# Performance work log

Measured on AMD Instinct MI355X. Metric: run time of the kernel, lower is better.

## Reference

```python
import jax, jax.numpy as jnp
import numpy as np


def setup_inputs() -> dict:
    key = jax.random.key(0)
    k1, k2 = jax.random.split(key)
    x = jax.random.normal(k1, (4, 4096, 128), dtype=jnp.float32)
    kernel = jax.random.normal(k2, (3, 128, 64), dtype=jnp.float32)
    return {"x": x, "kernel": kernel}


def reference(x, kernel):
    # QKV projections: x [B,N,Din] @ kernel[i] [Din,Dout] -> [B,N,Dout]
    WQ = jnp.einsum('bnd,de->bne', x, kernel[0])
    WK = jnp.einsum('bnd,de->bne', x, kernel[1])
    WV = jnp.einsum('bnd,de->bne', x, kernel[2])
    d_out = WV.shape[-1]
    # scaled dot-product scores [B,N,N]
    scores = jnp.einsum('bqe,bke->bqk', WQ, WK) / jnp.sqrt(jnp.float32(d_out))
    attn = jax.nn.softmax(scores, axis=-1)
    return jnp.einsum('bqk,bke->bqe', attn, WV)
```

## Files before the change

kernel.cpp:

```cpp
#include <hip/hip_runtime.h>


typedef __attribute__((ext_vector_type(8))) short bf16x8;
typedef __attribute__((ext_vector_type(16))) float f32x16;
typedef __attribute__((ext_vector_type(4))) unsigned u32x4;
typedef unsigned short us;

__device__ __forceinline__ us f2bf(float f) {
  unsigned u = __builtin_bit_cast(unsigned, f);
  u += 0x7FFFu + ((u >> 16) & 1u);
  return (us)(u >> 16);
}
__device__ __forceinline__ float bf2f(us h) {
  unsigned u = ((unsigned)h) << 16;
  return __builtin_bit_cast(float, u);
}
__device__ __forceinline__ f32x16 mfma(bf16x8 a, bf16x8 b, f32x16 c) {
  return __builtin_amdgcn_mfma_f32_32x32x16_bf16(a, b, c, 0, 0, 0);
}
__device__ __forceinline__ unsigned pk2t(float a, float b) {
  return __builtin_amdgcn_perm(__builtin_bit_cast(unsigned, b),
                               __builtin_bit_cast(unsigned, a), 0x07060302u);
}
__device__ __forceinline__ void dma16(const us* g, us* l) {
  __builtin_amdgcn_global_load_lds(
      (const __attribute__((address_space(1))) unsigned*)g,
      (__attribute__((address_space(3))) unsigned*)l, 16, 0, 0);
}
#define EXP2(x) __builtin_amdgcn_exp2f(x)

#define NSEG 16
#define ITERS 4

__global__ __launch_bounds__(256, 1) void wprep_kernel(
    const float* __restrict__ w, us* __restrict__ Wbh, us* __restrict__ Wbl)
{
  const int i = blockIdx.x * 256 + threadIdx.x;
  if (i >= 24576) return;
  const int p = i >> 13, d = (i & 8191) >> 6, e = i & 63;
  float v = w[i];
  if (p == 0) v *= 0.18033688011112042f;
  const us hi = f2bf(v);
  const us lo = f2bf(v - bf2f(hi));
  const int g = (p * 64 + e) >> 5, ks = d >> 4, hh = (d >> 3) & 1, j = d & 7;
  const int o = ((g * 8 + ks) * 2 + hh) * 256 + (e & 31) * 8 + j;
  Wbh[o] = hi;
  Wbl[o] = lo;
}

__global__ __launch_bounds__(384, 1) void qkv_kernel(
    const float* __restrict__ x,
    const us* __restrict__ Wbh, const us* __restrict__ Wbl,
    us* __restrict__ Qhi, us* __restrict__ Qlo,
    us* __restrict__ Kbh, us* __restrict__ Kbl, us* __restrict__ Vb)
{
  __shared__ unsigned ttile[32 * 193];
  const int t = threadIdx.x;
  const int rb = blockIdx.x;
  const int wid = t >> 6, lane = t & 63;
  const int l31 = lane & 31, h = lane >> 5;
  const int rbase = rb * 32;
  const float* xrow = x + (size_t)(rbase + l31) * 128;

  f32x16 acc = {};
  #pragma unroll
  for (int ks = 0; ks < 8; ++ks) {
    const int d0 = ks * 16 + h * 8;
    const float4 xa = *(const float4*)(xrow + d0);
    const float4 xb = *(const float4*)(xrow + d0 + 4);
    const float xv[8] = {xa.x, xa.y, xa.z, xa.w, xb.x, xb.y, xb.z, xb.w};
    bf16x8 ah, al;
    #pragma unroll
    for (int j = 0; j < 8; ++j) {
      us hi = f2bf(xv[j]);
      ah[j] = (short)hi;
      al[j] = (short)f2bf(xv[j] - bf2f(hi));
    }
    const int wo = ((wid * 8 + ks) * 2 + h) * 256 + l31 * 8;
    bf16x8 bh = *(const bf16x8*)(Wbh + wo);
    bf16x8 bl = *(const bf16x8*)(Wbl + wo);
    acc = mfma(ah, bh, acc);
    acc = mfma(al, bh, acc);
    acc = mfma(ah, bl, acc);
  }

  #pragma unroll
  for (int r = 0; r < 16; ++r) {
    const int rl = (r & 3) + 8 * (r >> 2) + 4 * h;
    float v = acc[r];
    us hi = f2bf(v);
    us lo = f2bf(v - bf2f(hi));
    ttile[rl * 193 + wid * 32 + l31] = (unsigned)hi | ((unsigned)lo << 16);
  }
  __syncthreads();

  if (t < 64) {
    const int row = t >> 1, cb = (t & 1) * 32;
    const int grow = rbase + row;
    unsigned hw[16], lw[16];
    #pragma unroll
    for (int j = 0; j < 16; ++j) {
      unsigned a = ttile[row * 193 + cb + 2 * j];
      unsigned bv = ttile[row * 193 + cb + 2 * j + 1];
      hw[j] = (a & 0xffffu) | (bv << 16);
      lw[j] = (a >> 16) | (bv & 0xffff0000u);
    }
    #pragma unroll
    for (int j = 0; j < 4; ++j) {
      uint4 hv = {hw[4 * j], hw[4 * j + 1], hw[4 * j + 2], hw[4 * j + 3]};
      uint4 lv = {lw[4 * j], lw[4 * j + 1], lw[4 * j + 2], lw[4 * j + 3]};
      *(uint4*)(Qhi + (size_t)grow * 64 + cb + 8 * j) = hv;
      *(uint4*)(Qlo + (size_t)grow * 64 + cb + 8 * j) = lv;
    }
  } else if (t < 192) {
    const int bb = rbase >> 12;
    const int kt = (rbase & 4095) >> 6;
    const int m = (rbase >> 5) & 1;
    const size_t kbb = (size_t)bb * 262144 + (size_t)kt * 4096 + m * 256;
    #pragma unroll
    for (int i2 = 0; i2 < 2; ++i2) {
      const int c = (t - 64) + 128 * i2;
      const int r = c & 31, hh = (c >> 5) & 1, ks = c >> 6;
      unsigned hw[4], lw[4];
      #pragma unroll
      for (int j = 0; j < 4; ++j) {
        unsigned a = ttile[r * 193 + 64 + 16 * ks + 8 * hh + 2 * j];
        unsigned bv = ttile[r * 193 + 64 + 16 * ks + 8 * hh + 2 * j + 1];
        hw[j] = (a & 0xffffu) | (bv << 16);
        lw[j] = (a >> 16) | (bv & 0xffff0000u);
      }
      const size_t off = kbb + (size_t)(ks * 4 + 2 * hh) * 256 + r * 8;
      uint4 hv = {hw[0], hw[1], hw[2], hw[3]};
      uint4 lv = {lw[0], lw[1], lw[2], lw[3]};
      *(uint4*)(Kbh + off) = hv;
      *(uint4*)(Kbl + off) = lv;
    }
  } else if (t < 320) {
    const int bb = rbase >> 12;
    const int nb = rbase & 4095;
    #pragma unroll
    for (int i2 = 0; i2 < 2; ++i2) {
      const int c = (t - 192) + 128 * i2;
      const int e = c >> 2, nc = c & 3;
      unsigned p[4];
      #pragma unroll
      for (int j = 0; j < 4; ++j) {
        unsigned a = ttile[(nc * 8 + 2 * j) * 193 + 128 + e];
        unsigned bv = ttile[(nc * 8 + 2 * j + 1) * 193 + 128 + e];
        p[j] = (a & 0xffffu) | (bv << 16);
      }
      uint4 pv = {p[0], p[1], p[2], p[3]};
      const int n0 = nb + nc * 8;
      const int kt = n0 >> 6, sub = n0 & 63;
      const int ks = sub >> 4, hh = (sub >> 3) & 1;
      const int dt = e >> 5, lv = e & 31;
      *(uint4*)(Vb + (size_t)bb * 262144 +
                ((((kt * 4 + ks) * 2 + hh) * 2 + dt) * 256 + lv * 8)) = pv;
    }
  }
}

__global__ __launch_bounds__(256, 3) void attn_kernel(
    const us* __restrict__ Qhi, const us* __restrict__ Qlo,
    const us* __restrict__ Kbh, const us* __restrict__ Kbl,
    const us* __restrict__ Vb,
    us* __restrict__ Opart, float* __restrict__ Mpart,
    float* __restrict__ Lpart)
{
  __shared__ us stage[2][12288];
  __shared__ float alds[4][32];

  const int bx = blockIdx.x;
  const int xc = bx & 7, b = xc >> 1;
  const int idx = ((bx >> 3) << 1) | (xc & 1);
  const int seg = idx & (NSEG - 1), qg = idx >> 4;
  const int t = threadIdx.x;
  const int wid = t >> 6, lane = t & 63;
  const int l31 = lane & 31, h = lane >> 5;
  const int q0 = qg * 128 + wid * 32;
  const int u = (b * 4096 + q0) >> 5;
  const size_t pb = (size_t)u * NSEG + seg;

  bf16x8 qh[4], ql[4];
  {
    const size_t rg = (size_t)(b * 4096 + q0 + l31) * 64;
    #pragma unroll
    for (int ks = 0; ks < 4; ++ks) {
      qh[ks] = *(const bf16x8*)(Qhi + rg + ks * 16 + h * 8);
      ql[ks] = *(const bf16x8*)(Qlo + rg + ks * 16 + h * 8);
    }
  }
  const size_t kbase = (size_t)b * 262144;

  {
    const size_t kb0 = kbase + (size_t)(seg * ITERS) * 4096;
    #pragma unroll
    for (int i = 0; i < 6; ++i) {
      const int c = wid * 6 + i;
      const us* src = (c < 8)  ? Kbh + kb0 + c * 512
                    : (c < 16) ? Kbl + kb0 + (c - 8) * 512
                               : Vb  + kb0 + (c - 16) * 512;
      dma16(src + lane * 8, &stage[0][c * 512]);
    }
  }
  __syncthreads();

  f32x16 o[2] = {};
  float mrun = -__builtin_inff();
  float lrun = 0.f;

  for (int it = 0; it < ITERS; ++it) {
    const int cur = it & 1;
    const us* sb = &stage[cur][0];

    if (it + 1 < ITERS) {
      const size_t kbn = kbase + (size_t)(seg * ITERS + it + 1) * 4096;
      #pragma unroll
      for (int i = 0; i < 6; ++i) {
        const int c = wid * 6 + i;
        const us* src = (c < 8)  ? Kbh + kbn + c * 512
                      : (c < 16) ? Kbl + kbn + (c - 8) * 512
                                 : Vb  + kbn + (c - 16) * 512;
        dma16(src + lane * 8, &stage[cur ^ 1][c * 512]);
      }
    }

    f32x16 s[2] = {};
    #pragma unroll
    for (int ks = 0; ks < 4; ++ks) {
      #pragma unroll
      for (int m = 0; m < 2; ++m) {
        const int ko = (ks * 4 + 2 * h + m) * 256 + l31 * 8;
        const bf16x8 ah = *(const bf16x8*)(sb + ko);
        const bf16x8 al = *(const bf16x8*)(sb + 4096 + ko);
        s[m] = mfma(ah, qh[ks], s[m]);
        s[m] = mfma(al, qh[ks], s[m]);
        s[m] = mfma(ah, ql[ks], s[m]);
      }
    }

    float vm = -__builtin_inff();
    #pragma unroll
    for (int r = 0; r < 16; ++r)
      vm = fmaxf(vm, fmaxf(s[0][r], s[1][r]));
    vm = fmaxf(vm, __shfl_xor(vm, 32));

    if (!__all(vm <= mrun - 24.f)) {
      const float mnew = (vm > mrun + 0.5f) ? vm : mrun;
      const float alpha = EXP2(mrun - mnew);
      float sum = 0.f;
      unsigned pp[2][8];
      #pragma unroll
      for (int m = 0; m < 2; ++m) {
        #pragma unroll
        for (int p = 0; p < 8; ++p) {
          const float p0 = EXP2(s[m][2 * p] - mnew);
          const float p1 = EXP2(s[m][2 * p + 1] - mnew);
          sum += p0 + p1;
          pp[m][p] = pk2t(p0, p1);
        }
      }
      sum += __shfl_xor(sum, 32);
      lrun = lrun * alpha + sum;
      mrun = mnew;

      if (__any(alpha != 1.f)) {
        if (!h) alds[wid][l31] = alpha;
        #pragma unroll
        for (int g = 0; g < 4; ++g) {
          const float4 af4 = *(const float4*)(&alds[wid][8 * g + 4 * h]);
          #pragma unroll
          for (int rr = 0; rr < 4; ++rr) {
            const int r = 4 * g + rr;
            const float a = (rr == 0) ? af4.x : (rr == 1) ? af4.y
                           : (rr == 2) ? af4.z : af4.w;
            o[0][r] *= a;
            o[1][r] *= a;
          }
        }
      }

      #pragma unroll
      for (int ks = 0; ks < 4; ++ks) {
        const int vo = 8192 + (ks * 4 + 2 * h) * 256 + l31 * 8;
        const bf16x8 vf0 = *(const bf16x8*)(sb + vo);
        const bf16x8 vf1 = *(const bf16x8*)(sb + vo + 256);
        const int m = ks >> 1, base = 4 * (ks & 1);
        const unsigned x0 = pp[m][base + 0], x1 = pp[m][base + 1];
        const unsigned x2 = pp[m][base + 2], x3 = pp[m][base + 3];
        const unsigned sA = h ? x0 : x2;
        const unsigned sB = h ? x1 : x3;
        const unsigned rA = (unsigned)__shfl_xor((int)sA, 32);
        const unsigned rB = (unsigned)__shfl_xor((int)sB, 32);
        u32x4 wv;
        wv.x = h ? rA : x0;
        wv.y = h ? rB : x1;
        wv.z = h ? x2 : rA;
        wv.w = h ? x3 : rB;
        const bf16x8 af = __builtin_bit_cast(bf16x8, wv);
        o[0] = mfma(af, vf0, o[0]);
        o[1] = mfma(af, vf1, o[1]);
      }
    }

    __syncthreads();
  }

  float* fw = ((float*)&stage[0][0]) + wid * (32 * 34);
  #pragma unroll
  for (int dt = 0; dt < 2; ++dt) {
    #pragma unroll
    for (int r = 0; r < 16; ++r) {
      const int qrow = (r & 3) + 8 * (r >> 2) + 4 * h;
      fw[qrow * 34 + l31] = o[dt][r];
    }
    #pragma unroll
    for (int jj = 0; jj < 2; ++jj) {
      const int chunk = lane + 64 * jj;
      const int rw = chunk >> 2, part = chunk & 3;
      const float* src = &fw[rw * 34 + part * 8];
      float2 a0 = *(const float2*)(src + 0);
      float2 a1 = *(const float2*)(src + 2);
      float2 a2 = *(const float2*)(src + 4);
      float2 a3 = *(const float2*)(src + 6);
      uint4 pkv;
      pkv.x = pk2t(a0.x, a0.y);
      pkv.y = pk2t(a1.x, a1.y);
      pkv.z = pk2t(a2.x, a2.y);
      pkv.w = pk2t(a3.x, a3.y);
      *(uint4*)(Opart + pb * 2048 + (size_t)rw * 64 + dt * 32 + part * 8) =
          pkv;
    }
  }
  if (!h) {
    Mpart[pb * 32 + l31] = mrun;
    Lpart[pb * 32 + l31] = lrun;
  }
}

__global__ __launch_bounds__(256, 1) void merge_kernel(
    const us* __restrict__ Opart, const float* __restrict__ Mpart,
    const float* __restrict__ Lpart, float* __restrict__ out)
{
  const int tg = blockIdx.x * 256 + threadIdx.x;
  const int q = tg >> 3, dc = (tg & 7) * 8;
  const int u = q >> 5, ql = q & 31;
  const int base = u * NSEG;
  float M = -__builtin_inff();
  #pragma unroll
  for (int s = 0; s < NSEG; ++s)
    M = fmaxf(M, Mpart[(size_t)(base + s) * 32 + ql]);
  float acc[8] = {};
  float den = 0.f;
  #pragma unroll
  for (int s = 0; s < NSEG; ++s) {
    const float wgt = EXP2(Mpart[(size_t)(base + s) * 32 + ql] - M);
    den += wgt * Lpart[(size_t)(base + s) * 32 + ql];
    const uint4 r = *(const uint4*)(Opart + (size_t)(base + s) * 2048 +
                                    ql * 64 + dc);
    const unsigned rw[4] = {r.x, r.y, r.z, r.w};
    #pragma unroll
    for (int j = 0; j < 4; ++j) {
      acc[2 * j]     += wgt * bf2f((us)(rw[j] & 0xffffu));
      acc[2 * j + 1] += wgt * bf2f((us)(rw[j] >> 16));
    }
  }
  const float inv = 1.f / den;
  float4 r0 = {acc[0] * inv, acc[1] * inv, acc[2] * inv, acc[3] * inv};
  float4 r1 = {acc[4] * inv, acc[5] * inv, acc[6] * inv, acc[7] * inv};
  *(float4*)(out + (size_t)q * 64 + dc) = r0;
  *(float4*)(out + (size_t)q * 64 + dc + 4) = r1;
}

extern "C" void kernel_launch(void* const* d_in, const int* in_sizes, int n_in,
                              void* d_out, int out_size, void* d_ws,
                              size_t ws_size, hipStream_t stream)
{
  const float* x = (const float*)d_in[0];
  const float* w = (const float*)d_in[1];
  float* out = (float*)d_out;
  char* ws = (char*)d_ws;

  const size_t T = 2097152;
  us* Qhi = (us*)(ws + 0 * T);
  us* Qlo = (us*)(ws + 1 * T);
  us* Kbh = (us*)(ws + 2 * T);
  us* Kbl = (us*)(ws + 3 * T);
  us* Vb  = (us*)(ws + 4 * T);
  us* Wbh = (us*)(ws + 5 * T);
  us* Wbl = (us*)(ws + 5 * T + 49152);
  char* pbase = ws + 5 * T + 98304;
  us* Opart = (us*)pbase;
  float* Mpart = (float*)(pbase + 33554432);
  float* Lpart = (float*)(pbase + 33554432 + 1048576);

  hipLaunchKernelGGL(wprep_kernel, dim3(96), dim3(256), 0, stream,
                     w, Wbh, Wbl);
  hipLaunchKernelGGL(qkv_kernel, dim3(512), dim3(384), 0, stream,
                     x, Wbh, Wbl, Qhi, Qlo, Kbh, Kbl, Vb);
  hipLaunchKernelGGL(attn_kernel, dim3(2048), dim3(256), 0, stream,
                     Qhi, Qlo, Kbh, Kbl, Vb, Opart, Mpart, Lpart);
  hipLaunchKernelGGL(merge_kernel, dim3(512), dim3(256), 0, stream,
                     Opart, Mpart, Lpart, out);
}
```

Measured before the change: 122.1 us.

## Use permlane32 swap for P transpose, raise priority around MFMA blocks, split reductions

Replaces the two cross-half shuffles and selects that rebuild the P operand with v_permlane32_swap_b32 instructions, which swap register halves directly without going through LDS-based ds_bpermute. Raises wave priority around the QK and PV MFMA loops so waves in matrix phases get issued preferentially over waves doing softmax. Splits the row-max and row-sum reductions into two independent chains to shorten dependency latency. The swap semantics must match the old select pattern exactly, and the priority hints may do nothing or disturb the interleaving between waves.

After: 122.1 us. Within noise of the previous version (-0.0%).

```diff
diff --git a/kernel.cpp b/kernel.cpp
--- a/kernel.cpp
+++ b/kernel.cpp
@@ -226,6 +226,7 @@
     }
 
     f32x16 s[2] = {};
+    __builtin_amdgcn_s_setprio(1);
     #pragma unroll
     for (int ks = 0; ks < 4; ++ks) {
       #pragma unroll
@@ -238,17 +239,22 @@
         s[m] = mfma(ah, ql[ks], s[m]);
       }
     }
-
-    float vm = -__builtin_inff();
-    #pragma unroll
-    for (int r = 0; r < 16; ++r)
-      vm = fmaxf(vm, fmaxf(s[0][r], s[1][r]));
+    __builtin_amdgcn_s_setprio(0);
+
+    float va = fmaxf(s[0][0], s[1][0]);
+    float vb = fmaxf(s[0][1], s[1][1]);
+    #pragma unroll
+    for (int r = 2; r < 16; r += 2) {
+      va = fmaxf(va, fmaxf(s[0][r], s[1][r]));
+      vb = fmaxf(vb, fmaxf(s[0][r + 1], s[1][r + 1]));
+    }
+    float vm = fmaxf(va, vb);
     vm = fmaxf(vm, __shfl_xor(vm, 32));
 
     if (!__all(vm <= mrun - 24.f)) {
       const float mnew = (vm > mrun + 0.5f) ? vm : mrun;
       const float alpha = EXP2(mrun - mnew);
-      float sum = 0.f;
+      float sm0 = 0.f, sm1 = 0.f;
       unsigned pp[2][8];
       #pragma unroll
       for (int m = 0; m < 2; ++m) {
@@ -256,10 +262,12 @@
         for (int p = 0; p < 8; ++p) {
           const float p0 = EXP2(s[m][2 * p] - mnew);
           const float p1 = EXP2(s[m][2 * p + 1] - mnew);
-          sum += p0 + p1;
+          sm0 += p0;
+          sm1 += p1;
           pp[m][p] = pk2t(p0, p1);
         }
       }
+      float sum = sm0 + sm1;
       sum += __shfl_xor(sum, 32);
       lrun = lrun * alpha + sum;
       mrun = mnew;
@@ -280,27 +288,27 @@
         }
       }
 
+      __builtin_amdgcn_s_setprio(1);
       #pragma unroll
       for (int ks = 0; ks < 4; ++ks) {
         const int vo = 8192 + (ks * 4 + 2 * h) * 256 + l31 * 8;
         const bf16x8 vf0 = *(const bf16x8*)(sb + vo);
         const bf16x8 vf1 = *(const bf16x8*)(sb + vo + 256);
         const int m = ks >> 1, base = 4 * (ks & 1);
-        const unsigned x0 = pp[m][base + 0], x1 = pp[m][base + 1];
-        const unsigned x2 = pp[m][base + 2], x3 = pp[m][base + 3];
-        const unsigned sA = h ? x0 : x2;
-        const unsigned sB = h ? x1 : x3;
-        const unsigned rA = (unsigned)__shfl_xor((int)sA, 32);
-        const unsigned rB = (unsigned)__shfl_xor((int)sB, 32);
+        unsigned wx = pp[m][base + 0], wz = pp[m][base + 2];
+        unsigned wy = pp[m][base + 1], ww = pp[m][base + 3];
+        asm("v_permlane32_swap_b32 %0, %1" : "+v"(wx), "+v"(wz));
+        asm("v_permlane32_swap_b32 %0, %1" : "+v"(wy), "+v"(ww));
         u32x4 wv;
-        wv.x = h ? rA : x0;
-        wv.y = h ? rB : x1;
-        wv.z = h ? x2 : rA;
-        wv.w = h ? x3 : rB;
+        wv.x = wx;
+        wv.y = wy;
+        wv.z = wz;
+        wv.w = ww;
         const bf16x8 af = __builtin_bit_cast(bf16x8, wv);
         o[0] = mfma(af, vf0, o[0]);
         o[1] = mfma(af, vf1, o[1]);
       }
+      __builtin_amdgcn_s_setprio(0);
     }
 
     __syncthreads();
```
